# Kernel optimization log

Measured on AMD Instinct MI355X. Metric: run time of the kernel, lower is better.

The kernel has to match this reference:

```python
import jax, jax.numpy as jnp
import numpy as np

B, T, N, C, H, K = 32, 12, 512, 2, 64, 3
P = C + H  # 66, GCN input feature dim


def _xavier(key, fan_in, fan_out):
    std = (2.0 / (fan_in + fan_out)) ** 0.5
    return jax.random.normal(key, (fan_in, fan_out), dtype=jnp.float32) * std


def setup_inputs() -> dict:
    key = jax.random.key(0)
    k1, k2, k3, k4 = jax.random.split(key, 4)
    # scale adjacency so K-hop aggregation stays O(1) in magnitude
    G = jax.random.normal(k1, (K, N, N), dtype=jnp.float32) * (1.0 / np.sqrt(N))
    x_seq = jax.random.normal(k2, (B, T, N, C), dtype=jnp.float32)
    init_h = jnp.zeros((B, N, H), dtype=jnp.float32)
    W_gate = _xavier(k3, K * P, 2 * H)
    b_gate = jnp.zeros((2 * H,), dtype=jnp.float32)
    W_update = _xavier(k4, K * P, H)
    b_update = jnp.zeros((H,), dtype=jnp.float32)
    return {"G": G, "x_seq": x_seq, "init_h": init_h,
            "W_gate": W_gate, "b_gate": b_gate,
            "W_update": W_update, "b_update": b_update}


def _gcn(G, x, W, b):
    # x: [B, N, P]; G: [K, N, N] -> support_cat: [B, N, K*P] (k-major, matching torch cat order)
    Bq, Nq, Pq = x.shape
    sup = jnp.einsum('kij,bjp->bikp', G, x).reshape(Bq, Nq, -1)
    return sup @ W + b


def _cell(G, x, h, Wg, bg, Wu, bu):
    combined = jnp.concatenate([x, h], axis=-1)             # [B,N,C+H]
    zr = jax.nn.sigmoid(_gcn(G, combined, Wg, bg))           # [B,N,2H]
    z, r = zr[..., :H], zr[..., H:]
    candidate = jnp.concatenate([x, r * h], axis=-1)
    hc = jnp.tanh(_gcn(G, candidate, Wu, bu))
    return (1.0 - z) * h + z * hc


def reference(G, x_seq, init_h, W_gate, b_gate, W_update, b_update):
    # scan over time (sequential GRU state dependency)
    xs = jnp.swapaxes(x_seq, 0, 1)  # [T,B,N,C]

    def step(h, x_t):
        h2 = _cell(G, x_t, h, W_gate, b_gate, W_update, b_update)
        return h2, None

    h_last, _ = jax.lax.scan(step, init_h, xs)
    return h_last  # [B,N,H] — last hidden state of the (single) layer
```

## Files before the change

kernel.cpp:

```cpp
#include <hip/hip_runtime.h>
#include <hip/hip_bf16.h>
#include <cmath>

#define NN 512
#define BB 32
#define HH 64
#define TT 12
#define KS 3

#define OFF_GHI   0
#define OFF_GLO   393216
#define OFF_GPK   786432
#define OFF_XTH   1572864
#define OFF_XTL   1769472
#define OFF_SX    1966080
#define OFF_HHI   3145728
#define OFF_HLO   3670016
#define OFF_RHHI  4194304
#define OFF_Z     4718592
#define OFF_WHGH  6291456
#define OFF_WHGL  6304256
#define OFF_WHUH  6317056
#define OFF_WHUL  6323456
#define OFF_WXG   6329856
#define OFF_WXU   6330624

typedef __attribute__((ext_vector_type(8))) short v8s;
typedef __attribute__((ext_vector_type(4))) float f32x4;
typedef __attribute__((ext_vector_type(4))) unsigned short u16x4;

__device__ __forceinline__ unsigned short f2bf(float f) {
  union { __hip_bfloat16 h; unsigned short u; } x;
  x.h = __float2bfloat16(f);
  return x.u;
}
__device__ __forceinline__ float bf2f(unsigned short u) {
  union { unsigned short u; __hip_bfloat16 h; } x;
  x.u = u;
  return __bfloat162float(x.h);
}

__device__ __forceinline__ int swz64(int j, int key) {
  return (j & ~63) | ((((j >> 3) & 7) ^ key) << 3) | (j & 7);
}

__device__ __forceinline__ void gl_lds16(const unsigned short* g, short* l) {
  __builtin_amdgcn_global_load_lds(
      (const __attribute__((address_space(1))) void*)g,
      (__attribute__((address_space(3))) void*)l, 16, 0, 0);
}

__device__ __forceinline__ float fast_tanh(float x) {
  float e = __expf(2.f * x);
  return 1.f - 2.f / (e + 1.f);
}


__global__ __launch_bounds__(256) void pack_g(const float* __restrict__ G,
                                              unsigned short* __restrict__ Ghi,
                                              unsigned short* __restrict__ Glo) {
  int idx = blockIdx.x * 256 + threadIdx.x;
  if (idx >= KS * NN * NN) return;
  int j = idx & 511;
  int i = (idx >> 9) & 511;
  float g = G[idx];
  unsigned short hi = f2bf(g);
  unsigned short lo = f2bf(g - bf2f(hi));
  size_t pos = (size_t)(idx >> 9) * 512 + swz64(j, i & 7);
  Ghi[pos] = hi;
  Glo[pos] = lo;
}

__global__ __launch_bounds__(256) void pack_g2(const float* __restrict__ G,
                                               unsigned short* __restrict__ Gpk) {
  int idx = blockIdx.x * 256 + threadIdx.x;
  if (idx >= 1536 * 64) return;
  int L = idx & 63;
  int frag = idx >> 6;
  int m = frag % 3;
  int kf = (frag / 3) & 1;
  int j0 = (frag / 6) & 7;
  int i0w = frag / 48;
  int w = i0w & 3, i0 = i0w >> 2;
  int R = w * 48 + m * 16 + (L & 15);
  int ksec = R >> 6;
  int i = i0 * 64 + (R & 63);
  int jb = j0 * 64 + kf * 32 + (L >> 4) * 8;
  unsigned short* dst = Gpk + (size_t)frag * 512 + L * 8;
#pragma unroll
  for (int e = 0; e < 8; ++e) dst[e] = f2bf(G[((size_t)ksec * NN + i) * NN + jb + e]);
}

__global__ __launch_bounds__(256) void prep_xt2(const float* __restrict__ x_seq,
                                                unsigned short* __restrict__ Xh,
                                                unsigned short* __restrict__ Xl) {
  int idx = blockIdx.x * 256 + threadIdx.x;
  if (idx >= 768 * NN) return;
  int j = idx & 511;
  int col = idx >> 9;
  int t = col >> 6;
  int b = (col & 63) >> 1;
  int c = col & 1;
  float v = x_seq[((size_t)(b * TT + t) * NN + j) * 2 + c];
  unsigned short hi = f2bf(v);
  size_t pos = (size_t)col * 512 + swz64(j, col & 7);
  Xh[pos] = hi;
  Xl[pos] = f2bf(v - bf2f(hi));
}

__global__ __launch_bounds__(256) void prep_h2(const float* __restrict__ init_h,
                                               unsigned short* __restrict__ Hhi,
                                               unsigned short* __restrict__ Hlo) {
  int idx = blockIdx.x * 256 + threadIdx.x;
  if (idx >= 2048 * NN) return;
  int i = idx & 511;
  int col = idx >> 9;
  int b = col >> 6;
  int p = col & 63;
  float h = init_h[((size_t)b * NN + i) * HH + p];
  unsigned short hi = f2bf(h);
  size_t pos = (size_t)col * 512 + swz64(i, col & 7);
  Hhi[pos] = hi;
  Hlo[pos] = f2bf(h - bf2f(hi));
}

__global__ __launch_bounds__(256) void pack_w(const float* __restrict__ Wg,
                                              const float* __restrict__ Wu,
                                              unsigned short* __restrict__ Whgh,
                                              unsigned short* __restrict__ Whgl,
                                              unsigned short* __restrict__ Whuh,
                                              unsigned short* __restrict__ Whul,
                                              float* __restrict__ Wxg,
                                              float* __restrict__ Wxu) {
  int idx = blockIdx.x * 256 + threadIdx.x;
  if (idx < 128 * 192) {
    int o = idx & 127, kq = idx >> 7;
    int k = kq >> 6, q = kq & 63;
    float v = Wg[(size_t)(k * 66 + 2 + q) * 128 + o];
    unsigned short hi = f2bf(v);
    Whgh[o * 200 + kq] = hi;
    Whgl[o * 200 + kq] = f2bf(v - bf2f(hi));
  } else if (idx < 36864) {
    int j = idx - 24576;
    int o = j & 63, kq = j >> 6;
    int k = kq >> 6, q = kq & 63;
    float v = Wu[(size_t)(k * 66 + 2 + q) * 64 + o];
    unsigned short hi = f2bf(v);
    Whuh[o * 200 + kq] = hi;
    Whul[o * 200 + kq] = f2bf(v - bf2f(hi));
  } else if (idx < 37632) {
    int j = idx - 36864;
    int o = j & 127, kc = j >> 7;
    Wxg[kc * 128 + o] = Wg[(size_t)((kc >> 1) * 66 + (kc & 1)) * 128 + o];
  } else if (idx < 38016) {
    int j = idx - 37632;
    int o = j & 63, kc = j >> 6;
    Wxu[kc * 64 + o] = Wu[(size_t)((kc >> 1) * 66 + (kc & 1)) * 64 + o];
  }
}

__global__ __launch_bounds__(256) void gemm_sx(const unsigned short* __restrict__ Ghi,
                                               const unsigned short* __restrict__ Glo,
                                               const unsigned short* __restrict__ Xh,
                                               const unsigned short* __restrict__ Xl,
                                               float* __restrict__ Sx2) {
  __shared__ __align__(16) short sA[64 * 64];
  __shared__ __align__(16) short sB[64 * 64];
  int tid = threadIdx.x;
  int L = tid & 63, w = tid >> 6;
  int wm = (w >> 1) * 32, wn = (w & 1) * 32;
  int i0 = blockIdx.y * 64;
  int c0 = blockIdx.x * 64;
  f32x4 acc[2][2];
#pragma unroll
  for (int m = 0; m < 2; ++m)
#pragma unroll
    for (int n = 0; n < 2; ++n) acc[m][n] = (f32x4)(0.f);

  for (int j0 = 0; j0 < 1536; j0 += 64) {
    const unsigned short* Asel = (j0 < 512 || j0 >= 1024) ? Ghi : Glo;
    const unsigned short* Bsel = (j0 < 1024) ? Xh : Xl;
    int jb = j0 & 511;
    __syncthreads();
#pragma unroll
    for (int u = 0; u < 2; ++u) {
      int r = w * 16 + u * 8;
      gl_lds16(Asel + (size_t)(i0 + r + (L >> 3)) * 512 + jb + (L & 7) * 8, sA + r * 64);
      gl_lds16(Bsel + (size_t)(c0 + r + (L >> 3)) * 512 + jb + (L & 7) * 8, sB + r * 64);
    }
    __syncthreads();
#pragma unroll
    for (int kf = 0; kf < 2; ++kf) {
      int kog = kf * 4 + (L >> 4);
      v8s af[2], bf[2];
#pragma unroll
      for (int m = 0; m < 2; ++m) {
        int row = wm + m * 16 + (L & 15);
        af[m] = *(const v8s*)(sA + row * 64 + ((kog ^ (row & 7)) << 3));
      }
#pragma unroll
      for (int n = 0; n < 2; ++n) {
        int row = wn + n * 16 + (L & 15);
        bf[n] = *(const v8s*)(sB + row * 64 + ((kog ^ (row & 7)) << 3));
      }
#pragma unroll
      for (int m = 0; m < 2; ++m)
#pragma unroll
        for (int n = 0; n < 2; ++n)
          acc[m][n] = __builtin_amdgcn_mfma_f32_16x16x32_bf16(af[m], bf[n], acc[m][n], 0, 0, 0);
    }
  }
#pragma unroll
  for (int m = 0; m < 2; ++m)
#pragma unroll
    for (int r = 0; r < 4; ++r)
#pragma unroll
      for (int n = 0; n < 2; ++n)
        Sx2[(size_t)(i0 + wm + m * 16 + (L >> 4) * 4 + r) * 768 + c0 + wn + n * 16 + (L & 15)] =
            acc[m][n][r];
}

template <int GATE>
__global__ __launch_bounds__(512, 2) void fused_step(
    const unsigned short* __restrict__ Gpk,
    const unsigned short* __restrict__ Bhi,
    const float* __restrict__ Sx2,
    const unsigned short* __restrict__ Whi,
    const unsigned short* __restrict__ Wlo,
    const float* __restrict__ Wx,
    const float* __restrict__ bias,
    const unsigned short* __restrict__ Hr_hi,
    const unsigned short* __restrict__ Hr_lo,
    unsigned short* __restrict__ Ohi,
    unsigned short* __restrict__ Olo,
    float* __restrict__ Z,
    float* __restrict__ out, int t) {
  constexpr int O = GATE ? 128 : 64;
  constexpr int N2 = GATE ? 2 : 1;
  __shared__ __align__(16) char smem[67584];
  short* sBh = (short*)smem;
  short* sS  = (short*)smem;
  float* sSx = (float*)(smem + 65536);

  int tid = threadIdx.x;
  int L = tid & 63, w = tid >> 6;
  int wm = w & 3, wn = w >> 2;
  int bid = blockIdx.x;
  int xcd = bid & 7, local = bid >> 3;
  int i0t = ((xcd & 3) << 1) | (local & 1);
  int b = (local >> 1) + ((xcd >> 2) << 4);
  int i0 = i0t * 64;
  int bcol = b * 64;
  const unsigned short* Ap = Gpk + (size_t)(i0t * 4 + wm) * 48 * 512;

#pragma unroll
  for (int u = 0; u < 8; ++u) {
    int col = w * 8 + u;
    gl_lds16(Bhi + (size_t)(bcol + col) * 512 + L * 8, sBh + col * 512);
  }
  for (int e = tid; e < 384; e += 512) {
    int il = e / 6, kc = e % 6;
    sSx[e] = Sx2[(size_t)((kc >> 1) * 512 + i0 + il) * 768 + t * 64 + b * 2 + (kc & 1)];
  }
  __syncthreads();

  f32x4 acc[3][2];
#pragma unroll
  for (int m = 0; m < 3; ++m)
#pragma unroll
    for (int n = 0; n < 2; ++n) acc[m][n] = (f32x4)(0.f);
#pragma unroll
  for (int it = 0; it < 8; ++it) {
    v8s ah[2][3];
#pragma unroll
    for (int kf = 0; kf < 2; ++kf)
#pragma unroll
      for (int m = 0; m < 3; ++m)
        ah[kf][m] = *(const v8s*)(Ap + (size_t)((it * 2 + kf) * 3 + m) * 512 + L * 8);
#pragma unroll
    for (int kf = 0; kf < 2; ++kf) {
      int jj = it * 64 + kf * 32 + (L >> 4) * 8;
      v8s bh[2];
#pragma unroll
      for (int n = 0; n < 2; ++n) {
        int col = wn * 32 + n * 16 + (L & 15);
        int off = col * 512 + ((jj & ~63) | (((((jj >> 3) & 7) ^ (col & 7))) << 3));
        bh[n] = *(const v8s*)(sBh + off);
      }
#pragma unroll
      for (int m = 0; m < 3; ++m)
#pragma unroll
        for (int n = 0; n < 2; ++n)
          acc[m][n] = __builtin_amdgcn_mfma_f32_16x16x32_bf16(ah[kf][m], bh[n], acc[m][n], 0, 0, 0);
    }
  }
  __syncthreads();

#pragma unroll
  for (int m = 0; m < 3; ++m)
#pragma unroll
    for (int n = 0; n < 2; ++n)
#pragma unroll
      for (int r = 0; r < 4; ++r) {
        int R = wm * 48 + m * 16 + (L >> 4) * 4 + r;
        int il = R & 63, kk = R >> 6;
        int p = wn * 32 + n * 16 + (L & 15);
        float v = acc[m][n][r];
        unsigned short hi = f2bf(v);
        sS[il * 408 + kk * 64 + p] = (short)hi;
        sS[il * 408 + 200 + kk * 64 + p] = (short)f2bf(v - bf2f(hi));
      }
  __syncthreads();

  if (w < 4) {
    int wne = w * (O / 4);
    f32x4 acc2[4][N2];
#pragma unroll
    for (int m = 0; m < 4; ++m)
#pragma unroll
      for (int n = 0; n < N2; ++n) acc2[m][n] = (f32x4)(0.f);
#pragma unroll
    for (int s = 0; s < 3; ++s) {
      const unsigned short* Wsrc = (s < 2) ? Whi : Wlo;
      int abase = (s == 1) ? 200 : 0;
#pragma unroll
      for (int f = 0; f < 6; ++f) {
        int k0 = f * 32 + (L >> 4) * 8;
        v8s af2[4], bf2[N2];
#pragma unroll
        for (int m = 0; m < 4; ++m)
          af2[m] = *(const v8s*)(sS + (m * 16 + (L & 15)) * 408 + abase + k0);
#pragma unroll
        for (int n = 0; n < N2; ++n)
          bf2[n] = *(const v8s*)(Wsrc + (size_t)(wne + n * 16 + (L & 15)) * 200 + k0);
#pragma unroll
        for (int m = 0; m < 4; ++m)
#pragma unroll
          for (int n = 0; n < N2; ++n)
            acc2[m][n] =
                __builtin_amdgcn_mfma_f32_16x16x32_bf16(af2[m], bf2[n], acc2[m][n], 0, 0, 0);
      }
    }

#pragma unroll
    for (int m = 0; m < 4; ++m) {
#pragma unroll
      for (int n = 0; n < N2; ++n) {
        int o = wne + n * 16 + (L & 15);
        int il0 = m * 16 + (L >> 4) * 4;
        float vals[4];
#pragma unroll
        for (int r = 0; r < 4; ++r) {
          float v = acc2[m][n][r] + bias[o];
#pragma unroll
          for (int kc = 0; kc < 6; ++kc) v += sSx[(il0 + r) * 6 + kc] * Wx[kc * O + o];
          vals[r] = v;
        }
        if (GATE) {
          float sg[4];
#pragma unroll
          for (int r = 0; r < 4; ++r) sg[r] = 1.f / (1.f + __expf(-vals[r]));
          if (o < 64) {
#pragma unroll
            for (int r = 0; r < 4; ++r)
              Z[((size_t)b * 512 + i0 + il0 + r) * 64 + o] = sg[r];
          } else {
            int col = bcol + (o - 64);
            size_t cb = (size_t)col * 512 + i0 + (((il0 >> 3) ^ (col & 7)) << 3) + (il0 & 7);
            u16x4 h4 = *(const u16x4*)(Hr_hi + cb);
            u16x4 l4 = *(const u16x4*)(Hr_lo + cb);
            u16x4 oh;
#pragma unroll
            for (int r = 0; r < 4; ++r) {
              float h = bf2f(h4[r]) + bf2f(l4[r]);
              oh[r] = f2bf(sg[r] * h);
            }
            *(u16x4*)(Ohi + cb) = oh;
          }
        } else {
          int col = bcol + o;
          size_t cb = (size_t)col * 512 + i0 + (((il0 >> 3) ^ (col & 7)) << 3) + (il0 & 7);
          u16x4 h4 = *(const u16x4*)(Hr_hi + cb);
          u16x4 l4 = *(const u16x4*)(Hr_lo + cb);
          u16x4 oh, ol;
#pragma unroll
          for (int r = 0; r < 4; ++r) {
            float hc = fast_tanh(vals[r]);
            float z = Z[((size_t)b * 512 + i0 + il0 + r) * 64 + o];
            float h = bf2f(h4[r]) + bf2f(l4[r]);
            float hn = (1.f - z) * h + z * hc;
            unsigned short hi = f2bf(hn);
            oh[r] = hi;
            ol[r] = f2bf(hn - bf2f(hi));
            if (t == TT - 1) out[((size_t)b * 512 + i0 + il0 + r) * 64 + o] = hn;
          }
          *(u16x4*)(Ohi + cb) = oh;
          *(u16x4*)(Olo + cb) = ol;
        }
      }
    }
  }
}

extern "C" void kernel_launch(void* const* d_in, const int* in_sizes, int n_in,
                              void* d_out, int out_size, void* d_ws, size_t ws_size,
                              hipStream_t stream) {
  const float* G      = (const float*)d_in[0];
  const float* x_seq  = (const float*)d_in[1];
  const float* init_h = (const float*)d_in[2];
  const float* Wg     = (const float*)d_in[3];
  const float* bg     = (const float*)d_in[4];
  const float* Wu     = (const float*)d_in[5];
  const float* bu     = (const float*)d_in[6];
  float* out = (float*)d_out;
  float* ws = (float*)d_ws;

  unsigned short* GHI  = (unsigned short*)(ws + OFF_GHI);
  unsigned short* GLO  = (unsigned short*)(ws + OFF_GLO);
  unsigned short* GPK  = (unsigned short*)(ws + OFF_GPK);
  unsigned short* Xh   = (unsigned short*)(ws + OFF_XTH);
  unsigned short* Xl   = (unsigned short*)(ws + OFF_XTL);
  float* Sx2           = ws + OFF_SX;
  unsigned short* Hhi  = (unsigned short*)(ws + OFF_HHI);
  unsigned short* Hlo  = (unsigned short*)(ws + OFF_HLO);
  unsigned short* RHhi = (unsigned short*)(ws + OFF_RHHI);
  float* Z             = ws + OFF_Z;
  unsigned short* Whgh = (unsigned short*)(ws + OFF_WHGH);
  unsigned short* Whgl = (unsigned short*)(ws + OFF_WHGL);
  unsigned short* Whuh = (unsigned short*)(ws + OFF_WHUH);
  unsigned short* Whul = (unsigned short*)(ws + OFF_WHUL);
  float* Wxg           = ws + OFF_WXG;
  float* Wxu           = ws + OFF_WXU;

  pack_g<<<3072, 256, 0, stream>>>(G, GHI, GLO);
  pack_g2<<<384, 256, 0, stream>>>(G, GPK);
  prep_xt2<<<1536, 256, 0, stream>>>(x_seq, Xh, Xl);
  prep_h2<<<4096, 256, 0, stream>>>(init_h, Hhi, Hlo);
  pack_w<<<149, 256, 0, stream>>>(Wg, Wu, Whgh, Whgl, Whuh, Whul, Wxg, Wxu);
  gemm_sx<<<dim3(12, 24), 256, 0, stream>>>(GHI, GLO, Xh, Xl, Sx2);

  for (int t = 0; t < TT; ++t) {
    fused_step<1><<<256, 512, 0, stream>>>(GPK, Hhi, Sx2, Whgh, Whgl, Wxg, bg,
                                           Hhi, Hlo, RHhi, RHhi, Z, out, t);
    fused_step<0><<<256, 512, 0, stream>>>(GPK, RHhi, Sx2, Whuh, Whul, Wxu, bu,
                                           Hhi, Hlo, Hhi, Hlo, Z, out, t);
  }
}
```

Baseline: 367.1 us.

## Merge prep kernels, drop G low split, prefetch A fragments, use all warps in epilogue

Merges the five packing kernels into one launch to cut launch overhead. Drops the low-order bf16 part of G in the Sx precompute, removing a third of that GEMM's K loop at some cost in accuracy. In fused_step it double-buffers the G fragment loads from global memory one iteration ahead. The second-stage MFMA and epilogue are spread across all 8 warps instead of 4, at the price of more registers.

```diff
diff --git a/kernel.cpp b/kernel.cpp
--- a/kernel.cpp
+++ b/kernel.cpp
@@ -9,7 +9,6 @@
 #define KS 3
 
 #define OFF_GHI   0
-#define OFF_GLO   393216
 #define OFF_GPK   786432
 #define OFF_XTH   1572864
 #define OFF_XTL   1769472
@@ -55,112 +54,90 @@
   return 1.f - 2.f / (e + 1.f);
 }
 
-
-__global__ __launch_bounds__(256) void pack_g(const float* __restrict__ G,
-                                              unsigned short* __restrict__ Ghi,
-                                              unsigned short* __restrict__ Glo) {
+__global__ __launch_bounds__(256) void prep_all(
+    const float* __restrict__ G, const float* __restrict__ x_seq,
+    const float* __restrict__ init_h, const float* __restrict__ Wg,
+    const float* __restrict__ Wu,
+    unsigned short* __restrict__ Ghi, unsigned short* __restrict__ Gpk,
+    unsigned short* __restrict__ Xh, unsigned short* __restrict__ Xl,
+    unsigned short* __restrict__ Hhi, unsigned short* __restrict__ Hlo,
+    unsigned short* __restrict__ Whgh, unsigned short* __restrict__ Whgl,
+    unsigned short* __restrict__ Whuh, unsigned short* __restrict__ Whul,
+    float* __restrict__ Wxg, float* __restrict__ Wxu) {
   int idx = blockIdx.x * 256 + threadIdx.x;
-  if (idx >= KS * NN * NN) return;
-  int j = idx & 511;
-  int i = (idx >> 9) & 511;
-  float g = G[idx];
-  unsigned short hi = f2bf(g);
-  unsigned short lo = f2bf(g - bf2f(hi));
-  size_t pos = (size_t)(idx >> 9) * 512 + swz64(j, i & 7);
-  Ghi[pos] = hi;
-  Glo[pos] = lo;
-}
-
-__global__ __launch_bounds__(256) void pack_g2(const float* __restrict__ G,
-                                               unsigned short* __restrict__ Gpk) {
-  int idx = blockIdx.x * 256 + threadIdx.x;
-  if (idx >= 1536 * 64) return;
-  int L = idx & 63;
-  int frag = idx >> 6;
-  int m = frag % 3;
-  int kf = (frag / 3) & 1;
-  int j0 = (frag / 6) & 7;
-  int i0w = frag / 48;
-  int w = i0w & 3, i0 = i0w >> 2;
-  int R = w * 48 + m * 16 + (L & 15);
-  int ksec = R >> 6;
-  int i = i0 * 64 + (R & 63);
-  int jb = j0 * 64 + kf * 32 + (L >> 4) * 8;
-  unsigned short* dst = Gpk + (size_t)frag * 512 + L * 8;
-#pragma unroll
-  for (int e = 0; e < 8; ++e) dst[e] = f2bf(G[((size_t)ksec * NN + i) * NN + jb + e]);
-}
-
-__global__ __launch_bounds__(256) void prep_xt2(const float* __restrict__ x_seq,
-                                                unsigned short* __restrict__ Xh,
-                                                unsigned short* __restrict__ Xl) {
-  int idx = blockIdx.x * 256 + threadIdx.x;
-  if (idx >= 768 * NN) return;
-  int j = idx & 511;
-  int col = idx >> 9;
-  int t = col >> 6;
-  int b = (col & 63) >> 1;
-  int c = col & 1;
-  float v = x_seq[((size_t)(b * TT + t) * NN + j) * 2 + c];
-  unsigned short hi = f2bf(v);
-  size_t pos = (size_t)col * 512 + swz64(j, col & 7);
-  Xh[pos] = hi;
-  Xl[pos] = f2bf(v - bf2f(hi));
-}
-
-__global__ __launch_bounds__(256) void prep_h2(const float* __restrict__ init_h,
-                                               unsigned short* __restrict__ Hhi,
-                                               unsigned short* __restrict__ Hlo) {
-  int idx = blockIdx.x * 256 + threadIdx.x;
-  if (idx >= 2048 * NN) return;
-  int i = idx & 511;
-  int col = idx >> 9;
-  int b = col >> 6;
-  int p = col & 63;
-  float h = init_h[((size_t)b * NN + i) * HH + p];
-  unsigned short hi = f2bf(h);
-  size_t pos = (size_t)col * 512 + swz64(i, col & 7);
-  Hhi[pos] = hi;
-  Hlo[pos] = f2bf(h - bf2f(hi));
-}
-
-__global__ __launch_bounds__(256) void pack_w(const float* __restrict__ Wg,
-                                              const float* __restrict__ Wu,
-                                              unsigned short* __restrict__ Whgh,
-                                              unsigned short* __restrict__ Whgl,
-                                              unsigned short* __restrict__ Whuh,
-                                              unsigned short* __restrict__ Whul,
-                                              float* __restrict__ Wxg,
-                                              float* __restrict__ Wxu) {
-  int idx = blockIdx.x * 256 + threadIdx.x;
-  if (idx < 128 * 192) {
-    int o = idx & 127, kq = idx >> 7;
-    int k = kq >> 6, q = kq & 63;
-    float v = Wg[(size_t)(k * 66 + 2 + q) * 128 + o];
+  if (idx < 786432) {
+    int j = idx & 511;
+    int i = (idx >> 9) & 511;
+    Ghi[(size_t)(idx >> 9) * 512 + swz64(j, i & 7)] = f2bf(G[idx]);
+  } else if (idx < 884736) {
+    int t = idx - 786432;
+    int L = t & 63;
+    int frag = t >> 6;
+    int m = frag % 3;
+    int kf = (frag / 3) & 1;
+    int j0 = (frag / 6) & 7;
+    int i0w = frag / 48;
+    int w = i0w & 3, i0 = i0w >> 2;
+    int R = w * 48 + m * 16 + (L & 15);
+    int ksec = R >> 6;
+    int i = i0 * 64 + (R & 63);
+    int jb = j0 * 64 + kf * 32 + (L >> 4) * 8;
+    unsigned short* dst = Gpk + (size_t)frag * 512 + L * 8;
+#pragma unroll
+    for (int e = 0; e < 8; ++e) dst[e] = f2bf(G[((size_t)ksec * NN + i) * NN + jb + e]);
+  } else if (idx < 1277952) {
+    int t2 = idx - 884736;
+    int j = t2 & 511;
+    int col = t2 >> 9;
+    int t = col >> 6;
+    int b = (col & 63) >> 1;
+    int c = col & 1;
+    float v = x_seq[((size_t)(b * TT + t) * NN + j) * 2 + c];
     unsigned short hi = f2bf(v);
-    Whgh[o * 200 + kq] = hi;
-    Whgl[o * 200 + kq] = f2bf(v - bf2f(hi));
-  } else if (idx < 36864) {
-    int j = idx - 24576;
-    int o = j & 63, kq = j >> 6;
-    int k = kq >> 6, q = kq & 63;
-    float v = Wu[(size_t)(k * 66 + 2 + q) * 64 + o];
-    unsigned short hi = f2bf(v);
-    Whuh[o * 200 + kq] = hi;
-    Whul[o * 200 + kq] = f2bf(v - bf2f(hi));
-  } else if (idx < 37632) {
-    int j = idx - 36864;
-    int o = j & 127, kc = j >> 7;
-    Wxg[kc * 128 + o] = Wg[(size_t)((kc >> 1) * 66 + (kc & 1)) * 128 + o];
-  } else if (idx < 38016) {
-    int j = idx - 37632;
-    int o = j & 63, kc = j >> 6;
-    Wxu[kc * 64 + o] = Wu[(size_t)((kc >> 1) * 66 + (kc & 1)) * 64 + o];
+    size_t pos = (size_t)col * 512 + swz64(j, col & 7);
+    Xh[pos] = hi;
+    Xl[pos] = f2bf(v - bf2f(hi));
+  } else if (idx < 2326528) {
+    int t2 = idx - 1277952;
+    int i = t2 & 511;
+    int col = t2 >> 9;
+    int b = col >> 6;
+    int p = col & 63;
+    float h = init_h[((size_t)b * NN + i) * HH + p];
+    unsigned short hi = f2bf(h);
+    size_t pos = (size_t)col * 512 + swz64(i, col & 7);
+    Hhi[pos] = hi;
+    Hlo[pos] = f2bf(h - bf2f(hi));
+  } else if (idx < 2364544) {
+    int j2 = idx - 2326528;
+    if (j2 < 24576) {
+      int o = j2 & 127, kq = j2 >> 7;
+      int k = kq >> 6, q = kq & 63;
+      float v = Wg[(size_t)(k * 66 + 2 + q) * 128 + o];
+      unsigned short hi = f2bf(v);
+      Whgh[o * 200 + kq] = hi;
+      Whgl[o * 200 + kq] = f2bf(v - bf2f(hi));
+    } else if (j2 < 36864) {
+      int j = j2 - 24576;
+      int o = j & 63, kq = j >> 6;
+      int k = kq >> 6, q = kq & 63;
+      float v = Wu[(size_t)(k * 66 + 2 + q) * 64 + o];
+      unsigned short hi = f2bf(v);
+      Whuh[o * 200 + kq] = hi;
+      Whul[o * 200 + kq] = f2bf(v - bf2f(hi));
+    } else if (j2 < 37632) {
+      int j = j2 - 36864;
+      int o = j & 127, kc = j >> 7;
+      Wxg[kc * 128 + o] = Wg[(size_t)((kc >> 1) * 66 + (kc & 1)) * 128 + o];
+    } else {
+      int j = j2 - 37632;
+      int o = j & 63, kc = j >> 6;
+      Wxu[kc * 64 + o] = Wu[(size_t)((kc >> 1) * 66 + (kc & 1)) * 64 + o];
+    }
   }
 }
 
 __global__ __launch_bounds__(256) void gemm_sx(const unsigned short* __restrict__ Ghi,
-                                               const unsigned short* __restrict__ Glo,
                                                const unsigned short* __restrict__ Xh,
                                                const unsigned short* __restrict__ Xl,
                                                float* __restrict__ Sx2) {
@@ -177,15 +154,14 @@
 #pragma unroll
     for (int n = 0; n < 2; ++n) acc[m][n] = (f32x4)(0.f);
 
-  for (int j0 = 0; j0 < 1536; j0 += 64) {
-    const unsigned short* Asel = (j0 < 512 || j0 >= 1024) ? Ghi : Glo;
-    const unsigned short* Bsel = (j0 < 1024) ? Xh : Xl;
+  for (int j0 = 0; j0 < 1024; j0 += 64) {
+    const unsigned short* Bsel = (j0 < 512) ? Xh : Xl;
     int jb = j0 & 511;
     __syncthreads();
 #pragma unroll
     for (int u = 0; u < 2; ++u) {
       int r = w * 16 + u * 8;
-      gl_lds16(Asel + (size_t)(i0 + r + (L >> 3)) * 512 + jb + (L & 7) * 8, sA + r * 64);
+      gl_lds16(Ghi + (size_t)(i0 + r + (L >> 3)) * 512 + jb + (L & 7) * 8, sA + r * 64);
       gl_lds16(Bsel + (size_t)(c0 + r + (L >> 3)) * 512 + jb + (L & 7) * 8, sB + r * 64);
     }
     __syncthreads();
@@ -236,7 +212,7 @@
     float* __restrict__ Z,
     float* __restrict__ out, int t) {
   constexpr int O = GATE ? 128 : 64;
-  constexpr int N2 = GATE ? 2 : 1;
+  constexpr int NF = GATE ? 4 : 2;
   __shared__ __align__(16) char smem[67584];
   short* sBh = (short*)smem;
   short* sS  = (short*)smem;
@@ -253,6 +229,13 @@
   int bcol = b * 64;
   const unsigned short* Ap = Gpk + (size_t)(i0t * 4 + wm) * 48 * 512;
 
+  v8s ah[2][3];
+#pragma unroll
+  for (int kf = 0; kf < 2; ++kf)
+#pragma unroll
+    for (int m = 0; m < 3; ++m)
+      ah[kf][m] = *(const v8s*)(Ap + (size_t)(kf * 3 + m) * 512 + L * 8);
+
 #pragma unroll
   for (int u = 0; u < 8; ++u) {
     int col = w * 8 + u;
@@ -271,12 +254,14 @@
     for (int n = 0; n < 2; ++n) acc[m][n] = (f32x4)(0.f);
 #pragma unroll
   for (int it = 0; it < 8; ++it) {
-    v8s ah[2][3];
-#pragma unroll
-    for (int kf = 0; kf < 2; ++kf)
-#pragma unroll
-      for (int m = 0; m < 3; ++m)
-        ah[kf][m] = *(const v8s*)(Ap + (size_t)((it * 2 + kf) * 3 + m) * 512 + L * 8);
+    v8s an[2][3];
+    if (it < 7) {
+#pragma unroll
+      for (int kf = 0; kf < 2; ++kf)
+#pragma unroll
+        for (int m = 0; m < 3; ++m)
+          an[kf][m] = *(const v8s*)(Ap + (size_t)(((it + 1) * 2 + kf) * 3 + m) * 512 + L * 8);
+    }
 #pragma unroll
     for (int kf = 0; kf < 2; ++kf) {
       int jj = it * 64 + kf * 32 + (L >> 4) * 8;
@@ -293,6 +278,10 @@
         for (int n = 0; n < 2; ++n)
           acc[m][n] = __builtin_amdgcn_mfma_f32_16x16x32_bf16(ah[kf][m], bh[n], acc[m][n], 0, 0, 0);
     }
+#pragma unroll
+    for (int kf = 0; kf < 2; ++kf)
+#pragma unroll
+      for (int m = 0; m < 3; ++m) ah[kf][m] = an[kf][m];
   }
   __syncthreads();
 
@@ -312,92 +301,78 @@
       }
   __syncthreads();
 
-  if (w < 4) {
-    int wne = w * (O / 4);
-    f32x4 acc2[4][N2];
-#pragma unroll
-    for (int m = 0; m < 4; ++m)
-#pragma unroll
-      for (int n = 0; n < N2; ++n) acc2[m][n] = (f32x4)(0.f);
-#pragma unroll
-    for (int s = 0; s < 3; ++s) {
-      const unsigned short* Wsrc = (s < 2) ? Whi : Wlo;
-      int abase = (s == 1) ? 200 : 0;
-#pragma unroll
-      for (int f = 0; f < 6; ++f) {
-        int k0 = f * 32 + (L >> 4) * 8;
-        v8s af2[4], bf2[N2];
-#pragma unroll
-        for (int m = 0; m < 4; ++m)
-          af2[m] = *(const v8s*)(sS + (m * 16 + (L & 15)) * 408 + abase + k0);
-#pragma unroll
-        for (int n = 0; n < N2; ++n)
-          bf2[n] = *(const v8s*)(Wsrc + (size_t)(wne + n * 16 + (L & 15)) * 200 + k0);
-#pragma unroll
-        for (int m = 0; m < 4; ++m)
-#pragma unroll
-          for (int n = 0; n < N2; ++n)
-            acc2[m][n] =
-                __builtin_amdgcn_mfma_f32_16x16x32_bf16(af2[m], bf2[n], acc2[m][n], 0, 0, 0);
-      }
-    }
-
-#pragma unroll
-    for (int m = 0; m < 4; ++m) {
-#pragma unroll
-      for (int n = 0; n < N2; ++n) {
-        int o = wne + n * 16 + (L & 15);
-        int il0 = m * 16 + (L >> 4) * 4;
-        float vals[4];
+  int me = w & 3, oh = w >> 2;
+  f32x4 acc2[NF];
+#pragma unroll
+  for (int n = 0; n < NF; ++n) acc2[n] = (f32x4)(0.f);
+#pragma unroll
+  for (int s = 0; s < 3; ++s) {
+    const unsigned short* Wsrc = (s < 2) ? Whi : Wlo;
+    int abase = (s == 1) ? 200 : 0;
+#pragma unroll
+    for (int f = 0; f < 6; ++f) {
+      int k0 = f * 32 + (L >> 4) * 8;
+      v8s af2 = *(const v8s*)(sS + (me * 16 + (L & 15)) * 408 + abase + k0);
+#pragma unroll
+      for (int n = 0; n < NF; ++n) {
+        v8s bf2 = *(const v8s*)(Wsrc + (size_t)(oh * (O / 2) + n * 16 + (L & 15)) * 200 + k0);
+        acc2[n] = __builtin_amdgcn_mfma_f32_16x16x32_bf16(af2, bf2, acc2[n], 0, 0, 0);
+      }
+    }
+  }
+
+#pragma unroll
+  for (int n = 0; n < NF; ++n) {
+    int o = oh * (O / 2) + n * 16 + (L & 15);
+    int il0 = me * 16 + (L >> 4) * 4;
+    float vals[4];
+#pragma unroll
+    for (int r = 0; r < 4; ++r) {
+      float v = acc2[n][r] + bias[o];
+#pragma unroll
+      for (int kc = 0; kc < 6; ++kc) v += sSx[(il0 + r) * 6 + kc] * Wx[kc * O + o];
+      vals[r] = v;
+    }
+    if (GATE) {
+      float sg[4];
+#pragma unroll
+      for (int r = 0; r < 4; ++r) sg[r] = 1.f / (1.f + __expf(-vals[r]));
+      if (oh == 0) {
+#pragma unroll
+        for (int r = 0; r < 4; ++r)
+          Z[((size_t)b * 512 + i0 + il0 + r) * 64 + o] = sg[r];
+      } else {
+        int col = bcol + (o - 64);
+        size_t cb = (size_t)col * 512 + i0 + (((il0 >> 3) ^ (col & 7)) << 3) + (il0 & 7);
+        u16x4 h4 = *(const u16x4*)(Hr_hi + cb);
+        u16x4 l4 = *(const u16x4*)(Hr_lo + cb);
+        u16x4 oh4;
 #pragma unroll
         for (int r = 0; r < 4; ++r) {
-          float v = acc2[m][n][r] + bias[o];
-#pragma unroll
-          for (int kc = 0; kc < 6; ++kc) v += sSx[(il0 + r) * 6 + kc] * Wx[kc * O + o];
-          vals[r] = v;
+          float h = bf2f(h4[r]) + bf2f(l4[r]);
+          oh4[r] = f2bf(sg[r] * h);
         }
-        if (GATE) {
-          float sg[4];
-#pragma unroll
-          for (int r = 0; r < 4; ++r) sg[r] = 1.f / (1.f + __expf(-vals[r]));
-          if (o < 64) {
-#pragma unroll
-            for (int r = 0; r < 4; ++r)
-              Z[((size_t)b * 512 + i0 + il0 + r) * 64 + o] = sg[r];
-          } else {
-            int col = bcol + (o - 64);
-            size_t cb = (size_t)col * 512 + i0 + (((il0 >> 3) ^ (col & 7)) << 3) + (il0 & 7);
-            u16x4 h4 = *(const u16x4*)(Hr_hi + cb);
-            u16x4 l4 = *(const u16x4*)(Hr_lo + cb);
-            u16x4 oh;
-#pragma unroll
-            for (int r = 0; r < 4; ++r) {
-              float h = bf2f(h4[r]) + bf2f(l4[r]);
-              oh[r] = f2bf(sg[r] * h);
-            }
-            *(u16x4*)(Ohi + cb) = oh;
-          }
-        } else {
-          int col = bcol + o;
-          size_t cb = (size_t)col * 512 + i0 + (((il0 >> 3) ^ (col & 7)) << 3) + (il0 & 7);
-          u16x4 h4 = *(const u16x4*)(Hr_hi + cb);
-          u16x4 l4 = *(const u16x4*)(Hr_lo + cb);
-          u16x4 oh, ol;
-#pragma unroll
-          for (int r = 0; r < 4; ++r) {
-            float hc = fast_tanh(vals[r]);
-            float z = Z[((size_t)b * 512 + i0 + il0 + r) * 64 + o];
-            float h = bf2f(h4[r]) + bf2f(l4[r]);
-            float hn = (1.f - z) * h + z * hc;
-            unsigned short hi = f2bf(hn);
-            oh[r] = hi;
-            ol[r] = f2bf(hn - bf2f(hi));
-            if (t == TT - 1) out[((size_t)b * 512 + i0 + il0 + r) * 64 + o] = hn;
-          }
-          *(u16x4*)(Ohi + cb) = oh;
-          *(u16x4*)(Olo + cb) = ol;
-        }
-      }
+        *(u16x4*)(Ohi + cb) = oh4;
+      }
+    } else {
+      int col = bcol + o;
+      size_t cb = (size_t)col * 512 + i0 + (((il0 >> 3) ^ (col & 7)) << 3) + (il0 & 7);
+      u16x4 h4 = *(const u16x4*)(Hr_hi + cb);
+      u16x4 l4 = *(const u16x4*)(Hr_lo + cb);
+      u16x4 oh4, ol4;
+#pragma unroll
+      for (int r = 0; r < 4; ++r) {
+        float hc = fast_tanh(vals[r]);
+        float z = Z[((size_t)b * 512 + i0 + il0 + r) * 64 + o];
+        float h = bf2f(h4[r]) + bf2f(l4[r]);
+        float hn = (1.f - z) * h + z * hc;
+        unsigned short hi = f2bf(hn);
+        oh4[r] = hi;
+        ol4[r] = f2bf(hn - bf2f(hi));
+        if (t == TT - 1) out[((size_t)b * 512 + i0 + il0 + r) * 64 + o] = hn;
+      }
+      *(u16x4*)(Ohi + cb) = oh4;
+      *(u16x4*)(Olo + cb) = ol4;
     }
   }
 }
@@ -416,7 +391,6 @@
   float* ws = (float*)d_ws;
 
   unsigned short* GHI  = (unsigned short*)(ws + OFF_GHI);
-  unsigned short* GLO  = (unsigned short*)(ws + OFF_GLO);
   unsigned short* GPK  = (unsigned short*)(ws + OFF_GPK);
   unsigned short* Xh   = (unsigned short*)(ws + OFF_XTH);
   unsigned short* Xl   = (unsigned short*)(ws + OFF_XTL);
@@ -432,12 +406,9 @@
   float* Wxg           = ws + OFF_WXG;
   float* Wxu           = ws + OFF_WXU;
 
-  pack_g<<<3072, 256, 0, stream>>>(G, GHI, GLO);
-  pack_g2<<<384, 256, 0, stream>>>(G, GPK);
-  prep_xt2<<<1536, 256, 0, stream>>>(x_seq, Xh, Xl);
-  prep_h2<<<4096, 256, 0, stream>>>(init_h, Hhi, Hlo);
-  pack_w<<<149, 256, 0, stream>>>(Wg, Wu, Whgh, Whgl, Whuh, Whul, Wxg, Wxu);
-  gemm_sx<<<dim3(12, 24), 256, 0, stream>>>(GHI, GLO, Xh, Xl, Sx2);
+  prep_all<<<9237, 256, 0, stream>>>(G, x_seq, init_h, Wg, Wu, GHI, GPK, Xh, Xl,
+                                     Hhi, Hlo, Whgh, Whgl, Whuh, Whul, Wxg, Wxu);
+  gemm_sx<<<dim3(12, 24), 256, 0, stream>>>(GHI, Xh, Xl, Sx2);
 
   for (int t = 0; t < TT; ++t) {
     fused_step<1><<<256, 512, 0, stream>>>(GPK, Hhi, Sx2, Whgh, Whgl, Wxg, bg,
```

Measured after the change: 402.8 us. +9.7%, slower.
